# Kernel tuning notes

Measured on AMD Instinct MI355X. Metric: run time of the kernel, lower is better.

Reference implementation:

```python
import jax, jax.numpy as jnp
import numpy as np

D_MODEL = 768
HEAD_SIZE = 64

def setup_inputs() -> dict:
    key = jax.random.key(0)
    ks = jax.random.split(key, 7)
    B, S = 8, 2048
    x = jax.random.normal(ks[0], (B, S, D_MODEL), dtype=jnp.float32)
    s = 1.0 / np.sqrt(D_MODEL)
    Wq = jax.random.uniform(ks[1], (D_MODEL, HEAD_SIZE), jnp.float32, -s, s)
    bq = jnp.zeros((HEAD_SIZE,), jnp.float32)
    Wk = jax.random.uniform(ks[2], (D_MODEL, HEAD_SIZE), jnp.float32, -s, s)
    bk = jnp.zeros((HEAD_SIZE,), jnp.float32)
    Wv = jax.random.uniform(ks[3], (D_MODEL, HEAD_SIZE), jnp.float32, -s, s)
    bv = jnp.zeros((HEAD_SIZE,), jnp.float32)
    return {"x": x, "Wq": Wq, "bq": bq, "Wk": Wk, "bk": bk, "Wv": Wv, "bv": bv}

def reference(x, Wq, bq, Wk, bk, Wv, bv):
    # Single attention head: softmax(Q K^T / sqrt(head_size)) V
    q = jnp.einsum('bsd,dh->bsh', x, Wq) + bq  # [B,S,H]
    k = jnp.einsum('bsd,dh->bsh', x, Wk) + bk
    v = jnp.einsum('bsd,dh->bsh', x, Wv) + bv
    scale = 1.0 / jnp.sqrt(jnp.array(HEAD_SIZE, dtype=x.dtype))
    scores = jnp.einsum('bqh,bkh->bqk', q, k) * scale  # [B,S,S]
    attn = jax.nn.softmax(scores, axis=-1)
    out = jnp.einsum('bqk,bkh->bqh', attn, v)  # [B,S,H]
    return out
```

## Files before the change

kernel.cpp:

```cpp
#include <hip/hip_runtime.h>
#include <math.h>

#define D_MODEL 768
#define HS 64
#define BATCH 8
#define SEQ 2048
#define QSCALE_LOG2E 0.1803368801f
#define KSPLIT 8
#define KCHUNK (SEQ / KSPLIT)
#define PM 32

typedef _Float16 half_t;
typedef __attribute__((ext_vector_type(8))) _Float16 half8;
typedef __attribute__((ext_vector_type(4))) float floatx4;

typedef const __attribute__((address_space(1))) void gas_void;
typedef __attribute__((address_space(3))) void las_void;
__device__ __forceinline__ void gl_lds16(const void* g, void* l) {
    __builtin_amdgcn_global_load_lds((gas_void*)g, (las_void*)l, 16, 0, 0);
}
__device__ __forceinline__ void waitcnt_all() {
    __builtin_amdgcn_s_waitcnt(0);
}
__device__ __forceinline__ float fast_exp2(float x) {
#if __has_builtin(__builtin_amdgcn_exp2f)
    return __builtin_amdgcn_exp2f(x);
#else
    return exp2f(x);
#endif
}

__global__ __launch_bounds__(256)
void wconv_kernel(const float* __restrict__ Wq, const float* __restrict__ Wk,
                  const float* __restrict__ Wv, half_t* __restrict__ Wt)
{
    __shared__ float lds[64][65];
    const int m = blockIdx.x / 12;
    const int k0 = (blockIdx.x % 12) * 64;
    const float* W = (m == 0) ? Wq : ((m == 1) ? Wk : Wv);
    const int tid = threadIdx.x;
#pragma unroll
    for (int ri = 0; ri < 4; ++ri) {
        int row = ri * 16 + (tid >> 4);
        int col = (tid & 15) * 4;
        float4 v = *(const float4*)(W + (size_t)(k0 + row) * HS + col);
        lds[row][col] = v.x; lds[row][col + 1] = v.y;
        lds[row][col + 2] = v.z; lds[row][col + 3] = v.w;
    }
    __syncthreads();
#pragma unroll
    for (int i = 0; i < 2; ++i) {
        int idx = i * 256 + tid;
        int h = idx >> 3;
        int kc = idx & 7;
        half8 o;
#pragma unroll
        for (int j = 0; j < 8; ++j) o[j] = (half_t)lds[kc * 8 + j][h];
        *(half8*)(Wt + (size_t)(m * HS + h) * D_MODEL + k0 + kc * 8) = o;
    }
}

__global__ __launch_bounds__(256)
void proj_kernel(const float* __restrict__ x, const half_t* __restrict__ Wt,
                 const float* __restrict__ bq, const float* __restrict__ bk,
                 const float* __restrict__ bv,
                 half_t* __restrict__ Qh, half_t* __restrict__ Kh,
                 half_t* __restrict__ Vt)
{
    __shared__ __align__(16) half_t xs[2][PM * 64];
    __shared__ __align__(16) half_t wtl[2][192 * 64];

    const int tid = threadIdx.x;
    const int w = tid >> 6;
    const int lane = tid & 63;
    const int l15 = lane & 15;
    const int quad = lane >> 4;
    const long row0 = (long)blockIdx.x * PM;

    floatx4 acc[2][3];
#pragma unroll
    for (int i = 0; i < 2; ++i)
#pragma unroll
        for (int j = 0; j < 3; ++j) acc[i][j] = (floatx4){0.f, 0.f, 0.f, 0.f};

    float4 xA[2], xB[2];

    auto loadx = [&](int k0, float4 (&v)[2]) {
        int r = tid >> 3, sc = tid & 7;
        int cg = sc ^ (r & 7);
        const float* p = x + (row0 + r) * D_MODEL + k0 + cg * 8;
        v[0] = *(const float4*)p;
        v[1] = *(const float4*)(p + 4);
    };
    auto stage_w = [&](int p, int k0) {
#pragma unroll
        for (int i = 0; i < 6; ++i) {
            int idx = i * 256 + tid;
            int r = idx >> 3, sc = idx & 7;
            int cg = sc ^ (r & 7);
            gl_lds16(Wt + (size_t)r * D_MODEL + k0 + cg * 8, &wtl[p][idx * 8]);
        }
    };

    auto step = [&](int it, float4 (&xc)[2], float4 (&xn)[2], int p) {
        {
            float4 a = xc[0], b = xc[1];
            half8 xh = (half8){(half_t)a.x, (half_t)a.y, (half_t)a.z, (half_t)a.w,
                               (half_t)b.x, (half_t)b.y, (half_t)b.z, (half_t)b.w};
            *(half8*)&xs[p][tid * 8] = xh;
        }
        waitcnt_all();
        __syncthreads();
        int kn = (it + 1 < 12) ? (it + 1) * 64 : 0;
        if (it + 1 < 12) stage_w(p ^ 1, kn);
        loadx(kn, xn);
#pragma unroll
        for (int kst = 0; kst < 2; ++kst) {
            half8 af[2];
#pragma unroll
            for (int mt = 0; mt < 2; ++mt) {
                int r = mt * 16 + l15;
                int slot = (kst * 4 + quad) ^ (r & 7);
                af[mt] = *(const half8*)&xs[p][r * 64 + slot * 8];
            }
#pragma unroll
            for (int nt = 0; nt < 3; ++nt) {
                int r = w * 48 + nt * 16 + l15;
                int slot = (kst * 4 + quad) ^ (r & 7);
                half8 bf = *(const half8*)&wtl[p][r * 64 + slot * 8];
#pragma unroll
                for (int mt = 0; mt < 2; ++mt)
                    acc[mt][nt] = __builtin_amdgcn_mfma_f32_16x16x32_f16(
                        af[mt], bf, acc[mt][nt], 0, 0, 0);
            }
        }
    };

    stage_w(0, 0);
    loadx(0, xA);
#pragma unroll
    for (int it = 0; it < 12; it += 2) {
        step(it,     xA, xB, 0);
        step(it + 1, xB, xA, 1);
    }

#pragma unroll
    for (int nt = 0; nt < 3; ++nt) {
        int nbase = w * 48 + nt * 16;
        int mm = nbase >> 6;
        int h = (nbase + l15) & 63;
        const float* bias = (mm == 0) ? bq : ((mm == 1) ? bk : bv);
        float bval = bias[h];
#pragma unroll
        for (int mt = 0; mt < 2; ++mt)
#pragma unroll
            for (int r = 0; r < 4; ++r) {
                long R = row0 + mt * 16 + quad * 4 + r;
                float fv = acc[mt][nt][r] + bval;
                if (mm == 0) {
                    Qh[R * HS + h] = (half_t)(fv * QSCALE_LOG2E);
                } else if (mm == 1) {
                    Kh[R * HS + h] = (half_t)fv;
                } else {
                    long bb = R >> 11, s = R & 2047;
                    Vt[(bb * HS + h) * SEQ + s] = (half_t)fv;
                }
            }
    }
}

__global__ __launch_bounds__(128)
void attn_kernel(const half_t* __restrict__ Qh, const half_t* __restrict__ Kh,
                 const half_t* __restrict__ Vt,
                 half_t* __restrict__ Opart, float* __restrict__ lpart)
{
    __shared__ __align__(16) half_t ks[2][64 * 64];

    const int tid = threadIdx.x;
    const int w = tid >> 6;
    const int lane = tid & 63;
    const int l15 = lane & 15;
    const int quad = lane >> 4;
    const int b = blockIdx.y;
    const int q0 = blockIdx.x * 128 + w * 64;
    const int kh = blockIdx.z;
    const int kk_begin = kh * KCHUNK;

    const half_t* Kb = Kh + (size_t)b * SEQ * HS;
    const half_t* Vb = Vt + (size_t)b * HS * SEQ;

    auto stage = [&](int p, int kk0) {
#pragma unroll
        for (int i = 0; i < 4; ++i) {
            int idx = i * 128 + tid;
            int r = idx >> 3, sc = idx & 7;
            int key = (r & 3) | ((r >> 1) & 4);
            int cg = sc ^ key;
            gl_lds16(Kb + (size_t)(kk0 + r) * HS + cg * 8, &ks[p][idx * 8]);
        }
    };

    stage(0, kk_begin);

    half8 qf[4][2];
#pragma unroll
    for (int mt = 0; mt < 4; ++mt)
#pragma unroll
        for (int hst = 0; hst < 2; ++hst)
            qf[mt][hst] = *(const half8*)(Qh + ((size_t)b * SEQ + q0 + mt * 16 + l15) * HS
                                          + hst * 32 + quad * 8);

    floatx4 oacc[4][4];
    float lsum[4];
#pragma unroll
    for (int mt = 0; mt < 4; ++mt) {
#pragma unroll
        for (int nt = 0; nt < 4; ++nt) oacc[mt][nt] = (floatx4){0.f, 0.f, 0.f, 0.f};
        lsum[mt] = 0.f;
    }

    for (int it = 0; it < KCHUNK / 64; ++it) {
        const int cur = it & 1;
        const int kk0 = kk_begin + it * 64;
        waitcnt_all();
        __syncthreads();
        if (it + 1 < KCHUNK / 64)
            stage(cur ^ 1, kk0 + 64);

        half8 vf[4][2];
#pragma unroll
        for (int nt = 0; nt < 4; ++nt)
#pragma unroll
            for (int kst = 0; kst < 2; ++kst)
                vf[nt][kst] = *(const half8*)(Vb + (size_t)(nt * 16 + l15) * SEQ
                                              + kk0 + kst * 32 + quad * 8);

        half8 kfr[4][2];
#pragma unroll
        for (int t = 0; t < 4; ++t) {
            int r = ((t >> 1) << 5) | ((l15 >> 2) << 3) | ((t & 1) << 2) | (l15 & 3);
            int key = (r & 3) | ((r >> 1) & 4);
#pragma unroll
            for (int hst = 0; hst < 2; ++hst) {
                int slot = (hst * 4 + quad) ^ key;
                kfr[t][hst] = *(const half8*)&ks[cur][r * 64 + slot * 8];
            }
        }

#pragma unroll
        for (int h2 = 0; h2 < 2; ++h2) {
            floatx4 sacc[2][4];
#pragma unroll
            for (int mtl = 0; mtl < 2; ++mtl)
#pragma unroll
                for (int t = 0; t < 4; ++t) sacc[mtl][t] = (floatx4){0.f, 0.f, 0.f, 0.f};
#pragma unroll
            for (int t = 0; t < 4; ++t)
#pragma unroll
                for (int hst = 0; hst < 2; ++hst)
#pragma unroll
                    for (int mtl = 0; mtl < 2; ++mtl)
                        sacc[mtl][t] = __builtin_amdgcn_mfma_f32_16x16x32_f16(
                            kfr[t][hst], qf[h2 * 2 + mtl][hst], sacc[mtl][t], 0, 0, 0);

#pragma unroll
            for (int mtl = 0; mtl < 2; ++mtl) {
                int mt = h2 * 2 + mtl;
                union { int i[4]; half8 h; } pa[2];
#pragma unroll
                for (int t = 0; t < 4; ++t)
#pragma unroll
                    for (int pr = 0; pr < 2; ++pr) {
                        float p0 = fast_exp2(sacc[mtl][t][pr * 2]);
                        float p1 = fast_exp2(sacc[mtl][t][pr * 2 + 1]);
                        lsum[mt] += p0 + p1;
                        union { _Float16 hh[2]; int ii; } u;
                        u.hh[0] = (half_t)p0;
                        u.hh[1] = (half_t)p1;
                        pa[t >> 1].i[(t & 1) * 2 + pr] = u.ii;
                    }
#pragma unroll
                for (int kst = 0; kst < 2; ++kst)
#pragma unroll
                    for (int nt = 0; nt < 4; ++nt)
                        oacc[mt][nt] = __builtin_amdgcn_mfma_f32_16x16x32_f16(
                            pa[kst].h, vf[nt][kst], oacc[mt][nt], 0, 0, 0);
            }
        }
    }

#pragma unroll
    for (int mt = 0; mt < 4; ++mt) {
        float s = lsum[mt];
        s += __shfl_xor(s, 16);
        s += __shfl_xor(s, 32);
        lsum[mt] = s;
    }

    size_t obase = ((size_t)kh * BATCH + b) * SEQ * HS;
#pragma unroll
    for (int mt = 0; mt < 4; ++mt)
#pragma unroll
        for (int nt = 0; nt < 4; ++nt)
#pragma unroll
            for (int r = 0; r < 4; ++r) {
                int row = q0 + mt * 16 + quad * 4 + r;
                Opart[obase + (size_t)row * HS + nt * 16 + l15] = (half_t)oacc[mt][nt][r];
            }
    if (lane < 16) {
#pragma unroll
        for (int mt = 0; mt < 4; ++mt) {
            int row = q0 + mt * 16 + l15;
            lpart[((size_t)kh * BATCH + b) * SEQ + row] = lsum[mt];
        }
    }
}

__global__ __launch_bounds__(256)
void combine_kernel(const half_t* __restrict__ Opart, const float* __restrict__ lpart,
                    float* __restrict__ out)
{
    const size_t NT = (size_t)BATCH * SEQ * HS;
    const size_t BS = (size_t)BATCH * SEQ;
    size_t e0 = ((size_t)blockIdx.x * 256 + threadIdx.x) * 8;
    size_t row = e0 / HS;
    float o[8] = {0, 0, 0, 0, 0, 0, 0, 0};
    float l = 0.f;
#pragma unroll
    for (int i = 0; i < KSPLIT; ++i) {
        half8 oi = *(const half8*)(Opart + (size_t)i * NT + e0);
#pragma unroll
        for (int j = 0; j < 8; ++j) o[j] += (float)oi[j];
        l += lpart[(size_t)i * BS + row];
    }
    float inv = 1.f / l;
    float4 a = {o[0] * inv, o[1] * inv, o[2] * inv, o[3] * inv};
    float4 c = {o[4] * inv, o[5] * inv, o[6] * inv, o[7] * inv};
    *(float4*)(out + e0) = a;
    *(float4*)(out + e0 + 4) = c;
}

extern "C" void kernel_launch(void* const* d_in, const int* in_sizes, int n_in,
                              void* d_out, int out_size, void* d_ws, size_t ws_size,
                              hipStream_t stream) {
    const float* x  = (const float*)d_in[0];
    const float* Wq = (const float*)d_in[1];
    const float* bq = (const float*)d_in[2];
    const float* Wk = (const float*)d_in[3];
    const float* bk = (const float*)d_in[4];
    const float* Wv = (const float*)d_in[5];
    const float* bv = (const float*)d_in[6];
    float* out = (float*)d_out;

    const size_t per = (size_t)BATCH * SEQ * HS;
    half_t* Qh = (half_t*)d_ws;
    half_t* Kh = Qh + per;
    half_t* Vt = Kh + per;
    half_t* Wt = Vt + per;
    half_t* Opart = Wt + 3 * HS * D_MODEL;
    float*  lpart = (float*)(Opart + (size_t)KSPLIT * per);

    wconv_kernel<<<dim3(36), dim3(256), 0, stream>>>(Wq, Wk, Wv, Wt);
    proj_kernel<<<dim3(BATCH * SEQ / PM), dim3(256), 0, stream>>>(
        x, Wt, bq, bk, bv, Qh, Kh, Vt);
    attn_kernel<<<dim3(SEQ / 128, BATCH, KSPLIT), dim3(128), 0, stream>>>(
        Qh, Kh, Vt, Opart, lpart);
    combine_kernel<<<dim3((BATCH * SEQ * HS) / (256 * 8)), dim3(256), 0, stream>>>(
        Opart, lpart, out);
}
```

Baseline: 132.8 us.

## Fuse split-K combine into attention kernel with in-block LDS reduction

Replaces the grid-level key split plus separate combine kernel with 512-thread blocks where each of 8 waves handles one key chunk for the same 64 query rows. Partial outputs and row sums are reduced through shared memory and written directly to the output, removing the fp16 partial-output round trip through global memory and one kernel launch. K tiles are now read directly from global memory per wave instead of being staged through double-buffered LDS. This drops the async prefetch and its swizzle, which may expose load latency. The grid also falls to 256 blocks.

```diff
diff --git a/kernel.cpp b/kernel.cpp
--- a/kernel.cpp
+++ b/kernel.cpp
@@ -169,38 +169,25 @@
     }
 }
 
-__global__ __launch_bounds__(128)
-void attn_kernel(const half_t* __restrict__ Qh, const half_t* __restrict__ Kh,
-                 const half_t* __restrict__ Vt,
-                 half_t* __restrict__ Opart, float* __restrict__ lpart)
+__global__ __launch_bounds__(512)
+void attn8_kernel(const half_t* __restrict__ Qh, const half_t* __restrict__ Kh,
+                  const half_t* __restrict__ Vt, float* __restrict__ out)
 {
-    __shared__ __align__(16) half_t ks[2][64 * 64];
+    __shared__ __align__(16) half_t osl[8][4096 + 32];
+    __shared__ float lsl[8][64];
 
     const int tid = threadIdx.x;
     const int w = tid >> 6;
     const int lane = tid & 63;
     const int l15 = lane & 15;
     const int quad = lane >> 4;
-    const int b = blockIdx.y;
-    const int q0 = blockIdx.x * 128 + w * 64;
-    const int kh = blockIdx.z;
-    const int kk_begin = kh * KCHUNK;
+    const int b  = blockIdx.x >> 5;
+    const int qt = blockIdx.x & 31;
+    const int q0 = qt * 64;
+    const int kk_begin = w * KCHUNK;
 
     const half_t* Kb = Kh + (size_t)b * SEQ * HS;
     const half_t* Vb = Vt + (size_t)b * HS * SEQ;
-
-    auto stage = [&](int p, int kk0) {
-#pragma unroll
-        for (int i = 0; i < 4; ++i) {
-            int idx = i * 128 + tid;
-            int r = idx >> 3, sc = idx & 7;
-            int key = (r & 3) | ((r >> 1) & 4);
-            int cg = sc ^ key;
-            gl_lds16(Kb + (size_t)(kk0 + r) * HS + cg * 8, &ks[p][idx * 8]);
-        }
-    };
-
-    stage(0, kk_begin);
 
     half8 qf[4][2];
 #pragma unroll
@@ -220,12 +207,7 @@
     }
 
     for (int it = 0; it < KCHUNK / 64; ++it) {
-        const int cur = it & 1;
         const int kk0 = kk_begin + it * 64;
-        waitcnt_all();
-        __syncthreads();
-        if (it + 1 < KCHUNK / 64)
-            stage(cur ^ 1, kk0 + 64);
 
         half8 vf[4][2];
 #pragma unroll
@@ -239,12 +221,10 @@
 #pragma unroll
         for (int t = 0; t < 4; ++t) {
             int r = ((t >> 1) << 5) | ((l15 >> 2) << 3) | ((t & 1) << 2) | (l15 & 3);
-            int key = (r & 3) | ((r >> 1) & 4);
-#pragma unroll
-            for (int hst = 0; hst < 2; ++hst) {
-                int slot = (hst * 4 + quad) ^ key;
-                kfr[t][hst] = *(const half8*)&ks[cur][r * 64 + slot * 8];
-            }
+#pragma unroll
+            for (int hst = 0; hst < 2; ++hst)
+                kfr[t][hst] = *(const half8*)(Kb + (size_t)(kk0 + r) * HS
+                                              + hst * 32 + quad * 8);
         }
 
 #pragma unroll
@@ -297,47 +277,32 @@
         lsum[mt] = s;
     }
 
-    size_t obase = ((size_t)kh * BATCH + b) * SEQ * HS;
 #pragma unroll
     for (int mt = 0; mt < 4; ++mt)
 #pragma unroll
         for (int nt = 0; nt < 4; ++nt)
 #pragma unroll
             for (int r = 0; r < 4; ++r) {
-                int row = q0 + mt * 16 + quad * 4 + r;
-                Opart[obase + (size_t)row * HS + nt * 16 + l15] = (half_t)oacc[mt][nt][r];
-            }
-    if (lane < 16) {
-#pragma unroll
-        for (int mt = 0; mt < 4; ++mt) {
-            int row = q0 + mt * 16 + l15;
-            lpart[((size_t)kh * BATCH + b) * SEQ + row] = lsum[mt];
-        }
-    }
-}
-
-__global__ __launch_bounds__(256)
-void combine_kernel(const half_t* __restrict__ Opart, const float* __restrict__ lpart,
-                    float* __restrict__ out)
-{
-    const size_t NT = (size_t)BATCH * SEQ * HS;
-    const size_t BS = (size_t)BATCH * SEQ;
-    size_t e0 = ((size_t)blockIdx.x * 256 + threadIdx.x) * 8;
-    size_t row = e0 / HS;
-    float o[8] = {0, 0, 0, 0, 0, 0, 0, 0};
-    float l = 0.f;
-#pragma unroll
-    for (int i = 0; i < KSPLIT; ++i) {
-        half8 oi = *(const half8*)(Opart + (size_t)i * NT + e0);
-#pragma unroll
-        for (int j = 0; j < 8; ++j) o[j] += (float)oi[j];
-        l += lpart[(size_t)i * BS + row];
-    }
-    float inv = 1.f / l;
-    float4 a = {o[0] * inv, o[1] * inv, o[2] * inv, o[3] * inv};
-    float4 c = {o[4] * inv, o[5] * inv, o[6] * inv, o[7] * inv};
-    *(float4*)(out + e0) = a;
-    *(float4*)(out + e0 + 4) = c;
+                int row = mt * 16 + quad * 4 + r;
+                osl[w][row * 64 + nt * 16 + l15] = (half_t)oacc[mt][nt][r];
+            }
+    if (quad == 0)
+#pragma unroll
+        for (int mt = 0; mt < 4; ++mt)
+            lsl[w][mt * 16 + l15] = lsum[mt];
+    __syncthreads();
+
+#pragma unroll
+    for (int i = 0; i < 8; ++i) {
+        int row = i * 8 + w;
+        float s = 0.f, l = 0.f;
+#pragma unroll
+        for (int s8 = 0; s8 < 8; ++s8) {
+            s += (float)osl[s8][row * 64 + lane];
+            l += lsl[s8][row];
+        }
+        out[((size_t)b * SEQ + q0 + row) * HS + lane] = s / l;
+    }
 }
 
 extern "C" void kernel_launch(void* const* d_in, const int* in_sizes, int n_in,
@@ -357,14 +322,10 @@
     half_t* Kh = Qh + per;
     half_t* Vt = Kh + per;
     half_t* Wt = Vt + per;
-    half_t* Opart = Wt + 3 * HS * D_MODEL;
-    float*  lpart = (float*)(Opart + (size_t)KSPLIT * per);
 
     wconv_kernel<<<dim3(36), dim3(256), 0, stream>>>(Wq, Wk, Wv, Wt);
     proj_kernel<<<dim3(BATCH * SEQ / PM), dim3(256), 0, stream>>>(
         x, Wt, bq, bk, bv, Qh, Kh, Vt);
-    attn_kernel<<<dim3(SEQ / 128, BATCH, KSPLIT), dim3(128), 0, stream>>>(
-        Qh, Kh, Vt, Opart, lpart);
-    combine_kernel<<<dim3((BATCH * SEQ * HS) / (256 * 8)), dim3(256), 0, stream>>>(
-        Opart, lpart, out);
-}
+    attn8_kernel<<<dim3(BATCH * (SEQ / 64)), dim3(512), 0, stream>>>(
+        Qh, Kh, Vt, out);
+}
```

Result: faster. 125.8 us (-5.3%).
